# Optimization experiments

Measured on AMD Instinct MI355X. Metric: run time of the kernel, lower is better.

Reference implementation:

```python
import jax, jax.numpy as jnp
import numpy as np

GRID_SIZE = 8
SCALE_SPLINE = 0.1
BATCH, IN_F, OUT_F = 2048, 1024, 1024


def setup_inputs() -> dict:
    key = jax.random.key(0)
    k1, k2, k3 = jax.random.split(key, 3)
    x = jax.random.normal(k1, (BATCH, IN_F), dtype=jnp.float32)
    # kaiming-uniform-ish scale for base linear weight
    bound = 1.0 / np.sqrt(IN_F)
    base_weight = jax.random.uniform(k2, (OUT_F, IN_F), dtype=jnp.float32,
                                     minval=-bound, maxval=bound)
    spline_coeff = 0.1 * jax.random.normal(k3, (OUT_F, IN_F, GRID_SIZE), dtype=jnp.float32)
    # grid buffer: identical linspace(-1,1,G+1) for every (out,in); keep 1-D
    grid = jnp.linspace(-1.0, 1.0, GRID_SIZE + 1, dtype=jnp.float32)
    return {"x": x, "base_weight": base_weight, "spline_coeff": spline_coeff, "grid": grid}


def reference(x, base_weight, spline_coeff, grid):
    # x: (B, I); base_weight: (O, I); spline_coeff: (O, I, G); grid: (G+1,)
    G = spline_coeff.shape[-1]
    base_out = x @ base_weight.T                       # (B, O)

    xc = jnp.clip(x, -1.0, 1.0)                        # (B, I)
    # bucketize: number of grid knots <= xc, minus 1, clamped to valid bin
    mask = xc[..., None] >= grid                       # (B, I, G+1)
    left_idx = jnp.clip(mask.sum(axis=-1) - 1, 0, G - 1)  # (B, I) int

    left_grid = grid[left_idx]                         # (B, I)
    right_grid = grid[left_idx + 1]                    # (B, I)
    denom = right_grid - left_grid
    denom = jnp.where(denom == 0, jnp.ones_like(denom), denom)
    weight = (xc - left_grid) / denom                  # (B, I)

    # coeff gather + weighted sum over in_features, expressed as a dense
    # contraction against a weight-scaled one-hot of the bin index:
    # spline_out[b,o] = sum_i spline_coeff[o,i,idx[b,i]] * weight[b,i]
    onehot_w = jax.nn.one_hot(left_idx, G, dtype=x.dtype) * weight[..., None]  # (B, I, G)
    spline_out = jnp.einsum('big,oig->bo', onehot_w, spline_coeff)             # (B, O)

    return base_out + SCALE_SPLINE * spline_out
```

## Files before the change

kernel.cpp:

```cpp
#include <hip/hip_runtime.h>
#include <stdint.h>

#define BATCH 2048
#define INF 1024
#define OUTF 1024
#define GRID_G 8
#define KTOT 9216

#define BM 128
#define BN 128
#define BK 32
#define SK 8
#define KC (KTOT / SK)
#define NKT (KC / BK)
#define MT (BATCH / BM)
#define NT (OUTF / BN)
#define CSLAB ((size_t)BATCH * OUTF)

typedef __attribute__((ext_vector_type(8))) short short8_t;
typedef __attribute__((ext_vector_type(4))) float f32x4_t;
typedef __attribute__((ext_vector_type(8))) unsigned short u16x8_t;

__device__ __forceinline__ unsigned short f2bf(float f) {
  unsigned int u = __float_as_uint(f);
  u += 0x7FFFu + ((u >> 16) & 1u);
  return (unsigned short)(u >> 16);
}

__device__ __forceinline__ void async16(void* lds, const void* g) {
  __builtin_amdgcn_global_load_lds(
      (const __attribute__((address_space(1))) void*)g,
      (__attribute__((address_space(3))) void*)lds, 16, 0, 0);
}

__global__ __launch_bounds__(256) void build_w_kernel(
    const float* __restrict__ bw, const float* __restrict__ coeff,
    unsigned short* __restrict__ wc) {
  int id = blockIdx.x * 256 + threadIdx.x;
  int row = id / (KTOT / 8);
  int k8 = id - row * (KTOT / 8);
  int k = k8 * 8;
  const float* src = (k < INF) ? (bw + (size_t)row * INF + k)
                               : (coeff + (size_t)row * (INF * GRID_G) + (k - INF));
  const float4* s4 = (const float4*)src;
  float4 a = s4[0], b = s4[1];
  u16x8_t v;
  v[0] = f2bf(a.x); v[1] = f2bf(a.y); v[2] = f2bf(a.z); v[3] = f2bf(a.w);
  v[4] = f2bf(b.x); v[5] = f2bf(b.y); v[6] = f2bf(b.z); v[7] = f2bf(b.w);
  *(u16x8_t*)(wc + (size_t)id * 8) = v;
}

__global__ __launch_bounds__(256) void build_a_kernel(
    const float* __restrict__ x, const float* __restrict__ grid,
    unsigned short* __restrict__ ac) {
  __shared__ float sg[GRID_G + 1];
  if (threadIdx.x <= GRID_G) sg[threadIdx.x] = grid[threadIdx.x];
  __syncthreads();
  int id = blockIdx.x * 256 + threadIdx.x;
  int b = id >> 10;
  int i = id & 1023;
  float xv = x[id];
  ac[(size_t)b * KTOT + i] = f2bf(xv);
  float xc = fminf(fmaxf(xv, -1.0f), 1.0f);
  int cnt = 0;
#pragma unroll
  for (int j = 0; j <= GRID_G; ++j) cnt += (xc >= sg[j]) ? 1 : 0;
  int idx = cnt - 1;
  idx = idx < 0 ? 0 : (idx > GRID_G - 1 ? GRID_G - 1 : idx);
  float left = sg[idx], right = sg[idx + 1];
  float denom = right - left;
  denom = (denom == 0.0f) ? 1.0f : denom;
  float w = (xc - left) / denom;
  unsigned short val = f2bf(0.1f * w);
  u16x8_t v;
#pragma unroll
  for (int g = 0; g < GRID_G; ++g) v[g] = (g == idx) ? val : (unsigned short)0;
  *(u16x8_t*)(ac + (size_t)b * KTOT + INF + (size_t)i * 8) = v;
}

__global__ __launch_bounds__(256) void gemm_kernel(
    const unsigned short* __restrict__ A, const unsigned short* __restrict__ W,
    unsigned short* __restrict__ P) {
  __shared__ unsigned short As[2][BM * BK];
  __shared__ unsigned short Bs[2][BN * BK];

  int bid = blockIdx.x;
  int sk = bid & 7;
  int t = bid >> 3;
  int mt = t >> 3;
  int nt = t & 7;

  int tid = threadIdx.x;
  int wave = tid >> 6;
  int lane = tid & 63;
  int wm = wave >> 1, wn = wave & 1;
  int lr = lane & 15, lk = lane >> 4;

  int srow = lane >> 2;
  int scol = (lane & 3) * 8;
  const unsigned short* ga0 = A + (size_t)(mt * BM + wave * 32 + 0 + srow) * KTOT + sk * KC + scol;
  const unsigned short* ga1 = A + (size_t)(mt * BM + wave * 32 + 16 + srow) * KTOT + sk * KC + scol;
  const unsigned short* gb0 = W + (size_t)(nt * BN + wave * 32 + 0 + srow) * KTOT + sk * KC + scol;
  const unsigned short* gb1 = W + (size_t)(nt * BN + wave * 32 + 16 + srow) * KTOT + sk * KC + scol;
  int lofs0 = (wave * 2 + 0) * 512;
  int lofs1 = (wave * 2 + 1) * 512;

  f32x4_t acc[4][4];
#pragma unroll
  for (int i2 = 0; i2 < 4; ++i2)
#pragma unroll
    for (int j2 = 0; j2 < 4; ++j2) acc[i2][j2] = f32x4_t{0.0f, 0.0f, 0.0f, 0.0f};

  async16(&As[0][lofs0], ga0);
  async16(&As[0][lofs1], ga1);
  async16(&Bs[0][lofs0], gb0);
  async16(&Bs[0][lofs1], gb1);

  for (int kt = 0; kt < NKT; ++kt) {
    int cur = kt & 1;
    __syncthreads();
    if (kt + 1 < NKT) {
      int nxt = cur ^ 1;
      const unsigned short* pa0 = ga0 + (kt + 1) * BK;
      const unsigned short* pa1 = ga1 + (kt + 1) * BK;
      const unsigned short* pb0 = gb0 + (kt + 1) * BK;
      const unsigned short* pb1 = gb1 + (kt + 1) * BK;
      async16(&As[nxt][lofs0], pa0);
      async16(&As[nxt][lofs1], pa1);
      async16(&Bs[nxt][lofs0], pb0);
      async16(&Bs[nxt][lofs1], pb1);
    }
    short8_t af[4], bf[4];
#pragma unroll
    for (int mi = 0; mi < 4; ++mi)
      af[mi] = *(const short8_t*)&As[cur][(wm * 64 + mi * 16 + lr) * BK + lk * 8];
#pragma unroll
    for (int ni = 0; ni < 4; ++ni)
      bf[ni] = *(const short8_t*)&Bs[cur][(wn * 64 + ni * 16 + lr) * BK + lk * 8];
#pragma unroll
    for (int mi = 0; mi < 4; ++mi)
#pragma unroll
      for (int ni = 0; ni < 4; ++ni)
        acc[mi][ni] = __builtin_amdgcn_mfma_f32_16x16x32_bf16(af[mi], bf[ni], acc[mi][ni], 0, 0, 0);
  }

  unsigned short* slab = P + (size_t)sk * CSLAB;
#pragma unroll
  for (int mi = 0; mi < 4; ++mi) {
#pragma unroll
    for (int ni = 0; ni < 4; ++ni) {
      int col = nt * BN + wn * 64 + ni * 16 + lr;
#pragma unroll
      for (int r = 0; r < 4; ++r) {
        int rowm = mt * BM + wm * 64 + mi * 16 + lk * 4 + r;
        slab[(size_t)rowm * OUTF + col] = f2bf(acc[mi][ni][r]);
      }
    }
  }
}

__global__ __launch_bounds__(256) void reduce_kernel(
    const unsigned short* __restrict__ P, float* __restrict__ out) {
  size_t base = ((size_t)blockIdx.x * 256 + threadIdx.x) * 8;
  float s[8];
#pragma unroll
  for (int j = 0; j < 8; ++j) s[j] = 0.0f;
#pragma unroll
  for (int k = 0; k < SK; ++k) {
    u16x8_t v = *(const u16x8_t*)(P + (size_t)k * CSLAB + base);
#pragma unroll
    for (int j = 0; j < 8; ++j)
      s[j] += __uint_as_float((unsigned int)v[j] << 16);
  }
  float4 lo = {s[0], s[1], s[2], s[3]};
  float4 hi = {s[4], s[5], s[6], s[7]};
  *(float4*)(out + base) = lo;
  *(float4*)(out + base + 4) = hi;
}

extern "C" void kernel_launch(void* const* d_in, const int* in_sizes, int n_in,
                              void* d_out, int out_size, void* d_ws, size_t ws_size,
                              hipStream_t stream) {
  const float* x = (const float*)d_in[0];
  const float* bw = (const float*)d_in[1];
  const float* coeff = (const float*)d_in[2];
  const float* grid = (const float*)d_in[3];
  float* out = (float*)d_out;

  unsigned short* Acat = (unsigned short*)d_ws;
  unsigned short* Wcat = Acat + (size_t)BATCH * KTOT;
  unsigned short* Part = Wcat + (size_t)OUTF * KTOT;

  build_w_kernel<<<OUTF * (KTOT / 8) / 256, 256, 0, stream>>>(bw, coeff, Wcat);
  build_a_kernel<<<BATCH * INF / 256, 256, 0, stream>>>(x, grid, Acat);
  gemm_kernel<<<SK * MT * NT, 256, 0, stream>>>(Acat, Wcat, Part);
  reduce_kernel<<<(int)(CSLAB / 8 / 256), 256, 0, stream>>>(Part, out);
}
```

Before: 84.28 us.

## Deepen GEMM prefetch with manual waitcnt, conflict-free LDS layout, and MFMA priority

Restructures the GEMM main loop so two K-tiles are in flight: the kernel issues loads two stages ahead and waits with explicit vmcnt counters instead of a full __syncthreads that drains all loads. The LDS tile layout changes so each 16-row fragment is stored contiguously in the order the MFMA operand reads use, which is meant to cut LDS bank conflicts. The MFMA block runs at raised wave priority, and the launch bounds ask for 4 blocks per CU. It adds a second barrier per iteration and relies on the hand-written waitcnt counts being correct.

```diff
diff --git a/kernel.cpp b/kernel.cpp
--- a/kernel.cpp
+++ b/kernel.cpp
@@ -78,7 +78,7 @@
   *(u16x8_t*)(ac + (size_t)b * KTOT + INF + (size_t)i * 8) = v;
 }
 
-__global__ __launch_bounds__(256) void gemm_kernel(
+__global__ __launch_bounds__(256, 4) void gemm_kernel(
     const unsigned short* __restrict__ A, const unsigned short* __restrict__ W,
     unsigned short* __restrict__ P) {
   __shared__ unsigned short As[2][BM * BK];
@@ -86,9 +86,9 @@
 
   int bid = blockIdx.x;
   int sk = bid & 7;
-  int t = bid >> 3;
-  int mt = t >> 3;
-  int nt = t & 7;
+  int t0 = bid >> 3;
+  int mt = t0 >> 3;
+  int nt = t0 & 7;
 
   int tid = threadIdx.x;
   int wave = tid >> 6;
@@ -96,14 +96,14 @@
   int wm = wave >> 1, wn = wave & 1;
   int lr = lane & 15, lk = lane >> 4;
 
-  int srow = lane >> 2;
-  int scol = (lane & 3) * 8;
-  const unsigned short* ga0 = A + (size_t)(mt * BM + wave * 32 + 0 + srow) * KTOT + sk * KC + scol;
-  const unsigned short* ga1 = A + (size_t)(mt * BM + wave * 32 + 16 + srow) * KTOT + sk * KC + scol;
-  const unsigned short* gb0 = W + (size_t)(nt * BN + wave * 32 + 0 + srow) * KTOT + sk * KC + scol;
-  const unsigned short* gb1 = W + (size_t)(nt * BN + wave * 32 + 16 + srow) * KTOT + sk * KC + scol;
-  int lofs0 = (wave * 2 + 0) * 512;
-  int lofs1 = (wave * 2 + 1) * 512;
+  int srow = wave * 16 + (lane & 15);
+  int scol = (lane >> 4) * 8;
+  const unsigned short* gA  = A + (size_t)(mt * BM + srow) * KTOT + sk * KC + scol;
+  const unsigned short* gA2 = gA + (size_t)64 * KTOT;
+  const unsigned short* gB  = W + (size_t)(nt * BN + srow) * KTOT + sk * KC + scol;
+  const unsigned short* gB2 = gB + (size_t)64 * KTOT;
+
+  int rlo = lk * 128 + lr * 8;
 
   f32x4_t acc[4][4];
 #pragma unroll
@@ -111,37 +111,48 @@
 #pragma unroll
     for (int j2 = 0; j2 < 4; ++j2) acc[i2][j2] = f32x4_t{0.0f, 0.0f, 0.0f, 0.0f};
 
-  async16(&As[0][lofs0], ga0);
-  async16(&As[0][lofs1], ga1);
-  async16(&Bs[0][lofs0], gb0);
-  async16(&Bs[0][lofs1], gb1);
-
-  for (int kt = 0; kt < NKT; ++kt) {
-    int cur = kt & 1;
-    __syncthreads();
-    if (kt + 1 < NKT) {
-      int nxt = cur ^ 1;
-      const unsigned short* pa0 = ga0 + (kt + 1) * BK;
-      const unsigned short* pa1 = ga1 + (kt + 1) * BK;
-      const unsigned short* pb0 = gb0 + (kt + 1) * BK;
-      const unsigned short* pb1 = gb1 + (kt + 1) * BK;
-      async16(&As[nxt][lofs0], pa0);
-      async16(&As[nxt][lofs1], pa1);
-      async16(&Bs[nxt][lofs0], pb0);
-      async16(&Bs[nxt][lofs1], pb1);
+#define STAGE_AB(bf_, tt) { \
+    int ko_ = (tt) * BK; \
+    unsigned short* da_ = &As[bf_][wave * 512]; \
+    async16(da_, gA + ko_); \
+    async16(da_ + 2048, gA2 + ko_); \
+    unsigned short* db_ = &Bs[bf_][wave * 512]; \
+    async16(db_, gB + ko_); \
+    async16(db_ + 2048, gB2 + ko_); }
+
+  STAGE_AB(0, 0)
+  STAGE_AB(1, 1)
+
+  for (int t = 0; t < NKT; ++t) {
+    int cur = t & 1;
+    if (t + 1 < NKT) {
+      asm volatile("s_waitcnt vmcnt(4)" ::: "memory");
+    } else {
+      asm volatile("s_waitcnt vmcnt(0)" ::: "memory");
     }
+    __builtin_amdgcn_s_barrier();
+    asm volatile("" ::: "memory");
+
     short8_t af[4], bf[4];
 #pragma unroll
     for (int mi = 0; mi < 4; ++mi)
-      af[mi] = *(const short8_t*)&As[cur][(wm * 64 + mi * 16 + lr) * BK + lk * 8];
+      af[mi] = *(const short8_t*)&As[cur][(wm * 4 + mi) * 512 + rlo];
 #pragma unroll
     for (int ni = 0; ni < 4; ++ni)
-      bf[ni] = *(const short8_t*)&Bs[cur][(wn * 64 + ni * 16 + lr) * BK + lk * 8];
+      bf[ni] = *(const short8_t*)&Bs[cur][(wn * 4 + ni) * 512 + rlo];
+
+    __builtin_amdgcn_s_setprio(1);
 #pragma unroll
     for (int mi = 0; mi < 4; ++mi)
 #pragma unroll
       for (int ni = 0; ni < 4; ++ni)
         acc[mi][ni] = __builtin_amdgcn_mfma_f32_16x16x32_bf16(af[mi], bf[ni], acc[mi][ni], 0, 0, 0);
+    __builtin_amdgcn_s_setprio(0);
+
+    asm volatile("s_waitcnt lgkmcnt(0)" ::: "memory");
+    __builtin_amdgcn_s_barrier();
+    asm volatile("" ::: "memory");
+    if (t + 2 < NKT) STAGE_AB(cur, t + 2)
   }
 
   unsigned short* slab = P + (size_t)sk * CSLAB;
```

After: 106.2 us. 1.26x slower.
